# Kernel tuning notes

Measured on AMD Instinct MI355X. Metric: run time of the kernel, lower is better.

The kernel has to match this reference:

```python
import jax, jax.numpy as jnp
import numpy as np

D_MODEL = 1024

def setup_inputs() -> dict:
    key = jax.random.key(0)
    k1, k2, k3, k4, k5 = jax.random.split(key, 5)
    x = jax.random.normal(k1, (4, 2048, D_MODEL), dtype=jnp.float32)
    # torch nn.Linear weights: [out_features, in_features]
    W_qkv = jax.random.normal(k2, (3 * D_MODEL, D_MODEL), dtype=jnp.float32) * (1.0 / np.sqrt(D_MODEL))
    b_qkv = jax.random.normal(k3, (3 * D_MODEL,), dtype=jnp.float32) * 0.01
    W_proj = jax.random.normal(k4, (D_MODEL, D_MODEL), dtype=jnp.float32) * (1.0 / np.sqrt(D_MODEL))
    b_proj = jax.random.normal(k5, (D_MODEL,), dtype=jnp.float32) * 0.01
    return {"x": x, "W_qkv": W_qkv, "b_qkv": b_qkv, "W_proj": W_proj, "b_proj": b_proj}

def reference(x, W_qkv, b_qkv, W_proj, b_proj):
    # qkv projection: x @ W.T + b  (torch Linear convention)
    qkv = jnp.einsum('bsd,ed->bse', x, W_qkv) + b_qkv  # [B,S,3D]
    q, k, v = jnp.split(qkv, 3, axis=-1)               # each [B,S,D]
    scale = 1.0 / jnp.sqrt(jnp.asarray(q.shape[-1], dtype=q.dtype))
    scores = jnp.einsum('bqd,bkd->bqk', q, k) * scale   # [B,S,S]
    attn = jax.nn.softmax(scores, axis=-1)
    out = jnp.einsum('bqk,bkd->bqd', attn, v)           # [B,S,D]
    return jnp.einsum('bsd,ed->bse', out, W_proj) + b_proj
```

## Files before the change

kernel.cpp:

```cpp
#include <hip/hip_runtime.h>
#include <stdint.h>
#include <stddef.h>


typedef __attribute__((ext_vector_type(8))) short bf16x8;
typedef __attribute__((ext_vector_type(4))) float f32x4;

__device__ __forceinline__ unsigned short f2bf(float f) {
  unsigned u = __float_as_uint(f);
  u += 0x7fffu + ((u >> 16) & 1u);
  return (unsigned short)(u >> 16);
}
__device__ __forceinline__ float bf2f(unsigned short h) {
  return __uint_as_float(((unsigned)h) << 16);
}

typedef const __attribute__((address_space(1))) void* gas_ptr;
typedef __attribute__((address_space(3))) void* las_ptr;

__device__ __forceinline__ void gload_lds16(const void* g, void* l) {
  __builtin_amdgcn_global_load_lds((gas_ptr)(uintptr_t)g,
                                   (las_ptr)(uint32_t)(uintptr_t)l, 16, 0, 0);
}

__device__ __forceinline__ f32x4 mfma16(bf16x8 a, bf16x8 b, f32x4 c) {
  return __builtin_amdgcn_mfma_f32_16x16x32_bf16(a, b, c, 0, 0, 0);
}

__global__ __launch_bounds__(256) void cvt_all(
    const float* __restrict__ x, unsigned short* __restrict__ xo,
    const float* __restrict__ wq, unsigned short* __restrict__ wqo,
    const float* __restrict__ wp, unsigned short* __restrict__ wpo) {
  const int NX = 8388608, NQ = 3145728, NP = 1048576;
  int i = (blockIdx.x * blockDim.x + threadIdx.x) * 4;
  int stride = gridDim.x * blockDim.x * 4;
  for (; i < NX + NQ + NP; i += stride) {
    const float* src;
    unsigned short* dst;
    int off;
    if (i < NX) { src = x; dst = xo; off = i; }
    else if (i < NX + NQ) { src = wq; dst = wqo; off = i - NX; }
    else { src = wp; dst = wpo; off = i - NX - NQ; }
    float4 v = *reinterpret_cast<const float4*>(src + off);
    ushort4 o;
    o.x = f2bf(v.x); o.y = f2bf(v.y); o.z = f2bf(v.z); o.w = f2bf(v.w);
    *reinterpret_cast<ushort4*>(dst + off) = o;
  }
}

__device__ __forceinline__ void stage_gf(const unsigned short* __restrict__ P,
                                         int ld, unsigned short* dst, int wid,
                                         int lane) {
#pragma unroll
  for (int c = 0; c < 4; ++c) {
    int s = (c * 4 + wid) * 64 + lane;
    int row = s >> 3, g = s & 7;
    gload_lds16(P + (size_t)row * ld + ((g ^ (row & 7)) * 8),
                dst + (c * 4 + wid) * 512);
  }
}

template <bool OUT_BF16, bool HAS_BIAS, bool EXPOUT, bool RINV, bool QKV>
__global__ __launch_bounds__(256, 2) void gf(
    const unsigned short* __restrict__ A, const unsigned short* __restrict__ B,
    void* __restrict__ Cv, void* __restrict__ Cv2,
    const float* __restrict__ bias,
    int K, int lda, int ldb, int ldc,
    long long strideA, long long strideB, long long strideC, float alpha) {
  __shared__ unsigned short lds[2][2][128 * 64];

  const int bz = blockIdx.z;
  const int gx = gridDim.x;
  int lin = blockIdx.y * gx + blockIdx.x;
  int bx, by;
  {
    const int nwg = gx * gridDim.y;
    const int q = nwg >> 3;
    lin = (lin & 7) * q + (lin >> 3);
    const int t = lin >> 6, r = lin & 63;
    const int tilesX = gx >> 3;
    bx = (t % tilesX) * 8 + (r & 7);
    by = (t / tilesX) * 8 + (r >> 3);
  }
  const int rowBase = by * 128;
  const int colBase = bx * 128;

  const unsigned short* Ap = A + (size_t)bz * (size_t)strideA + (size_t)rowBase * lda;
  const unsigned short* Bp = B + (size_t)bz * (size_t)strideB + (size_t)colBase * ldb;

  const int tid = threadIdx.x;
  const int wid = tid >> 6;
  const int lane = tid & 63;
  const int wr = wid >> 1;
  const int wc = wid & 1;
  const int fr = lane & 15;
  const int kgi = lane >> 4;

  const int nt = K >> 6;

  f32x4 acc[4][4] = {};
  f32x4 rsacc[4] = {};
  bf16x8 ones;
#pragma unroll
  for (int i = 0; i < 8; ++i) ones[i] = (short)0x3F80;

  stage_gf(Ap, lda, &lds[0][0][0], wid, lane);
  stage_gf(Bp, ldb, &lds[0][1][0], wid, lane);
  asm volatile("s_waitcnt vmcnt(0)" ::: "memory");
  __builtin_amdgcn_sched_barrier(0);
  __builtin_amdgcn_s_barrier();

  for (int t = 0; t < nt; ++t) {
    const int cur = t & 1;
    if (t + 1 < nt) {
      stage_gf(Ap + (size_t)(t + 1) * 64, lda, &lds[cur ^ 1][0][0], wid, lane);
      stage_gf(Bp + (size_t)(t + 1) * 64, ldb, &lds[cur ^ 1][1][0], wid, lane);
    }
    const unsigned short* sAc = &lds[cur][0][0];
    const unsigned short* sBc = &lds[cur][1][0];

    bf16x8 af[4][2], bv[4][2];
#pragma unroll
    for (int m = 0; m < 4; ++m) {
      int row = wr * 64 + m * 16 + fr;
      int r7 = row & 7;
      af[m][0] = *(const bf16x8*)&sAc[row * 64 + ((kgi ^ r7) * 8)];
      af[m][1] = *(const bf16x8*)&sAc[row * 64 + (((4 + kgi) ^ r7) * 8)];
    }
#pragma unroll
    for (int n = 0; n < 4; ++n) {
      int row = wc * 64 + n * 16 + fr;
      int r7 = row & 7;
      bv[n][0] = *(const bf16x8*)&sBc[row * 64 + ((kgi ^ r7) * 8)];
      bv[n][1] = *(const bf16x8*)&sBc[row * 64 + (((4 + kgi) ^ r7) * 8)];
    }
    asm volatile("s_waitcnt lgkmcnt(0)" ::: "memory");
    __builtin_amdgcn_sched_barrier(0);
    __builtin_amdgcn_s_setprio(1);
#pragma unroll
    for (int m = 0; m < 4; ++m)
#pragma unroll
      for (int n = 0; n < 4; ++n) {
        acc[m][n] = mfma16(af[m][0], bv[n][0], acc[m][n]);
        acc[m][n] = mfma16(af[m][1], bv[n][1], acc[m][n]);
      }
    if (RINV) {
#pragma unroll
      for (int m = 0; m < 4; ++m) {
        rsacc[m] = mfma16(af[m][0], ones, rsacc[m]);
        rsacc[m] = mfma16(af[m][1], ones, rsacc[m]);
      }
    }
    __builtin_amdgcn_s_setprio(0);
    __builtin_amdgcn_sched_barrier(0);
    asm volatile("s_waitcnt vmcnt(0)" ::: "memory");
    __builtin_amdgcn_sched_barrier(0);
    __builtin_amdgcn_s_barrier();
  }

  const int rg = (lane >> 4) * 4;
  const bool doTrans = QKV && (colBase >= 2048);

  if (doTrans) {
    unsigned short* cl = &lds[0][0][0];
#pragma unroll
    for (int m = 0; m < 4; ++m) {
      int rloc0 = wr * 64 + m * 16 + rg;
#pragma unroll
      for (int n = 0; n < 4; ++n) {
        int cloc = wc * 64 + n * 16 + fr;
        float bvs = HAS_BIAS ? bias[colBase + cloc] : 0.0f;
#pragma unroll
        for (int j = 0; j < 4; ++j) {
          float v = acc[m][n][j] * alpha + bvs;
          cl[cloc * 136 + rloc0 + j] = f2bf(v);
        }
      }
    }
    __syncthreads();
    const int b = rowBase >> 11;
    const int s0 = rowBase & 2047;
    const int dBase = colBase - 2048;
    unsigned short* Vt = reinterpret_cast<unsigned short*>(Cv2);
#pragma unroll
    for (int i = 0; i < 8; ++i) {
      int slot = i * 256 + tid;
      int d = slot >> 4, sg = slot & 15;
      bf16x8 v = *(const bf16x8*)&cl[d * 136 + sg * 8];
      *(bf16x8*)&Vt[((size_t)(b * 1024 + dBase + d)) * 2048 + s0 + sg * 8] = v;
    }
  } else if (OUT_BF16) {
    unsigned short* cl = &lds[0][0][0];
#pragma unroll
    for (int m = 0; m < 4; ++m) {
      int rloc0 = wr * 64 + m * 16 + rg;
      float rs4[4];
      if (RINV) {
#pragma unroll
        for (int j = 0; j < 4; ++j) rs4[j] = 1.0f / rsacc[m][j];
      }
#pragma unroll
      for (int n = 0; n < 4; ++n) {
        int cloc = wc * 64 + n * 16 + fr;
        float bvs = 0.0f;
        if (HAS_BIAS) bvs = bias[colBase + cloc];
#pragma unroll
        for (int j = 0; j < 4; ++j) {
          int row = rloc0 + j;
          float v = acc[m][n][j] * alpha;
          if (EXPOUT) v = __expf(v);
          else v += bvs;
          if (RINV) v *= rs4[j];
          int gW = cloc >> 3;
          int gS = (gW & 8) | ((gW & 7) ^ (row & 7));
          cl[row * 128 + gS * 8 + (cloc & 7)] = f2bf(v);
        }
      }
    }
    __syncthreads();
    unsigned short* Cb =
        reinterpret_cast<unsigned short*>(Cv) + (size_t)bz * (size_t)strideC;
#pragma unroll
    for (int i = 0; i < 8; ++i) {
      int slot = i * 256 + tid;
      int row = slot >> 4, g = slot & 15;
      int gS = (g & 8) | ((g & 7) ^ (row & 7));
      bf16x8 v = *(const bf16x8*)&cl[row * 128 + gS * 8];
      *(bf16x8*)&Cb[(size_t)(rowBase + row) * ldc + colBase + g * 8] = v;
    }
  } else {
    float* clf = reinterpret_cast<float*>(&lds[0][0][0]);
#pragma unroll
    for (int m = 0; m < 4; ++m) {
      int rloc0 = wr * 64 + m * 16 + rg;
#pragma unroll
      for (int n = 0; n < 4; ++n) {
        int cloc = wc * 64 + n * 16 + fr;
        float bvs = 0.0f;
        if (HAS_BIAS) bvs = bias[colBase + cloc];
#pragma unroll
        for (int j = 0; j < 4; ++j) {
          int row = rloc0 + j;
          float v = acc[m][n][j] * alpha + bvs;
          int gW = cloc >> 2;
          int gS = (gW & 24) | ((gW & 7) ^ (row & 7));
          clf[row * 128 + gS * 4 + (cloc & 3)] = v;
        }
      }
    }
    __syncthreads();
    float* Cf = reinterpret_cast<float*>(Cv) + (size_t)bz * (size_t)strideC;
#pragma unroll
    for (int i = 0; i < 16; ++i) {
      int slot = i * 256 + tid;
      int row = slot >> 5, g = slot & 31;
      int gS = (g & 24) | ((g & 7) ^ (row & 7));
      float4 v = *(const float4*)&clf[row * 128 + gS * 4];
      *(float4*)&Cf[(size_t)(rowBase + row) * ldc + colBase + g * 4] = v;
    }
  }
}

extern "C" void kernel_launch(void* const* d_in, const int* in_sizes, int n_in,
                              void* d_out, int out_size, void* d_ws, size_t ws_size,
                              hipStream_t stream) {
  const float* x     = (const float*)d_in[0];
  const float* Wqkv  = (const float*)d_in[1];
  const float* bqkv  = (const float*)d_in[2];
  const float* Wproj = (const float*)d_in[3];
  const float* bproj = (const float*)d_in[4];
  float* out = (float*)d_out;

  char* ws = (char*)d_ws;
  unsigned short* qk   = (unsigned short*)(ws + 0);
  unsigned short* xatt = (unsigned short*)(ws + 50331648);
  unsigned short* wq   = (unsigned short*)(ws + 67108864);
  unsigned short* wp   = (unsigned short*)(ws + 73400320);
  unsigned short* vt   = (unsigned short*)(ws + 75497472);
  unsigned short* sc   = (unsigned short*)(ws + 92274688);

  dim3 blk256(256);

  cvt_all<<<3072, blk256, 0, stream>>>(x, xatt, Wqkv, wq, Wproj, wp);

  gf<true, true, false, false, true><<<dim3(24, 64, 1), blk256, 0, stream>>>(
      xatt, wq, qk, vt, bqkv,
      1024, 1024, 1024, 2048, 0, 0, 0, 1.0f);

  gf<true, false, true, false, false><<<dim3(16, 16, 4), blk256, 0, stream>>>(
      qk, qk + 1024, sc, nullptr, nullptr,
      1024, 2048, 2048, 2048,
      2048LL * 2048, 2048LL * 2048, 2048LL * 2048, 0.03125f);

  gf<true, false, false, true, false><<<dim3(8, 16, 4), blk256, 0, stream>>>(
      sc, vt, xatt, nullptr, nullptr,
      2048, 2048, 2048, 1024,
      2048LL * 2048, 1024LL * 2048, 2048LL * 1024, 1.0f);

  gf<false, true, false, false, false><<<dim3(8, 64, 1), blk256, 0, stream>>>(
      xatt, wp, out, nullptr, bproj,
      1024, 1024, 1024, 1024, 0, 0, 0, 1.0f);
}
```

Before: 170.4 us.

## Add 256x256-tile 512-thread GEMM kernel for QKV and score stages

Introduces a new g256 kernel with 256x256 output tiles, 8 waves, and a 64 KB-per-buffer double-buffered LDS stage, and uses it for the QKV projection and the QK^T exp-score GEMM. The larger tile halves global/LDS traffic per FLOP compared with the 128x128 tiles. The V-transpose epilogue now uses a swizzled LDS layout instead of the padded one. The grid-swizzle is generalized to handle widths not divisible by 8. The cost is higher register pressure (8x4 accumulators per wave) and a much larger LDS footprint, 128 KB per block, which limits occupancy. Fewer blocks also risk tail effects, for example 384 blocks for QKV and 256 for scores.

```diff
diff --git a/kernel.cpp b/kernel.cpp
--- a/kernel.cpp
+++ b/kernel.cpp
@@ -48,26 +48,28 @@
   }
 }
 
-__device__ __forceinline__ void stage_gf(const unsigned short* __restrict__ P,
-                                         int ld, unsigned short* dst, int wid,
-                                         int lane) {
+__device__ __forceinline__ void stage_g256(const unsigned short* __restrict__ P,
+                                           int ld, unsigned short* dst,
+                                           int tid) {
+  const int wid = tid >> 6, lane = tid & 63;
 #pragma unroll
   for (int c = 0; c < 4; ++c) {
-    int s = (c * 4 + wid) * 64 + lane;
+    int s = c * 512 + tid;
     int row = s >> 3, g = s & 7;
     gload_lds16(P + (size_t)row * ld + ((g ^ (row & 7)) * 8),
-                dst + (c * 4 + wid) * 512);
-  }
-}
-
-template <bool OUT_BF16, bool HAS_BIAS, bool EXPOUT, bool RINV, bool QKV>
-__global__ __launch_bounds__(256, 2) void gf(
+                dst + (c * 512 + wid * 64) * 8);
+    (void)lane;
+  }
+}
+
+template <bool HAS_BIAS, bool EXPOUT, bool QKV_SPLIT>
+__global__ __launch_bounds__(512, 2) void g256(
     const unsigned short* __restrict__ A, const unsigned short* __restrict__ B,
     void* __restrict__ Cv, void* __restrict__ Cv2,
     const float* __restrict__ bias,
     int K, int lda, int ldb, int ldc,
     long long strideA, long long strideB, long long strideC, float alpha) {
-  __shared__ unsigned short lds[2][2][128 * 64];
+  __shared__ unsigned short lds[2][2][256 * 64];
 
   const int bz = blockIdx.z;
   const int gx = gridDim.x;
@@ -77,10 +79,193 @@
     const int nwg = gx * gridDim.y;
     const int q = nwg >> 3;
     lin = (lin & 7) * q + (lin >> 3);
-    const int t = lin >> 6, r = lin & 63;
-    const int tilesX = gx >> 3;
-    bx = (t % tilesX) * 8 + (r & 7);
-    by = (t / tilesX) * 8 + (r >> 3);
+    const int TW = (gx % 8 == 0) ? 8 : ((gx % 4 == 0) ? 4 : 1);
+    if (TW > 1) {
+      const int grp = TW * 8;
+      const int t = lin / grp, r = lin % grp;
+      const int tilesX = gx / TW;
+      bx = (t % tilesX) * TW + (r % TW);
+      by = (t / tilesX) * 8 + (r / TW);
+    } else {
+      bx = lin % gx; by = lin / gx;
+    }
+  }
+  const int rowBase = by * 256;
+  const int colBase = bx * 256;
+
+  const unsigned short* Ap = A + (size_t)bz * (size_t)strideA + (size_t)rowBase * lda;
+  const unsigned short* Bp = B + (size_t)bz * (size_t)strideB + (size_t)colBase * ldb;
+
+  const int tid = threadIdx.x;
+  const int wid = tid >> 6;
+  const int lane = tid & 63;
+  const int wr = wid >> 2;
+  const int wc = wid & 3;
+  const int fr = lane & 15;
+  const int kgi = lane >> 4;
+
+  const int nt = K >> 6;
+
+  f32x4 acc[8][4] = {};
+
+  stage_g256(Ap, lda, &lds[0][0][0], tid);
+  stage_g256(Bp, ldb, &lds[0][1][0], tid);
+  asm volatile("s_waitcnt vmcnt(0)" ::: "memory");
+  __builtin_amdgcn_sched_barrier(0);
+  __builtin_amdgcn_s_barrier();
+
+  for (int t = 0; t < nt; ++t) {
+    const int cur = t & 1;
+    if (t + 1 < nt) {
+      stage_g256(Ap + (size_t)(t + 1) * 64, lda, &lds[cur ^ 1][0][0], tid);
+      stage_g256(Bp + (size_t)(t + 1) * 64, ldb, &lds[cur ^ 1][1][0], tid);
+    }
+    const unsigned short* sAc = &lds[cur][0][0];
+    const unsigned short* sBc = &lds[cur][1][0];
+
+    bf16x8 af[8][2], bv[4][2];
+#pragma unroll
+    for (int m = 0; m < 8; ++m) {
+      int row = wr * 128 + m * 16 + fr;
+      int r7 = row & 7;
+      af[m][0] = *(const bf16x8*)&sAc[row * 64 + ((kgi ^ r7) * 8)];
+      af[m][1] = *(const bf16x8*)&sAc[row * 64 + (((4 + kgi) ^ r7) * 8)];
+    }
+#pragma unroll
+    for (int n = 0; n < 4; ++n) {
+      int row = wc * 64 + n * 16 + fr;
+      int r7 = row & 7;
+      bv[n][0] = *(const bf16x8*)&sBc[row * 64 + ((kgi ^ r7) * 8)];
+      bv[n][1] = *(const bf16x8*)&sBc[row * 64 + (((4 + kgi) ^ r7) * 8)];
+    }
+    asm volatile("s_waitcnt lgkmcnt(0)" ::: "memory");
+    __builtin_amdgcn_sched_barrier(0);
+    __builtin_amdgcn_s_setprio(1);
+#pragma unroll
+    for (int m = 0; m < 8; ++m)
+#pragma unroll
+      for (int n = 0; n < 4; ++n) {
+        acc[m][n] = mfma16(af[m][0], bv[n][0], acc[m][n]);
+        acc[m][n] = mfma16(af[m][1], bv[n][1], acc[m][n]);
+      }
+    __builtin_amdgcn_s_setprio(0);
+    __builtin_amdgcn_sched_barrier(0);
+    asm volatile("s_waitcnt vmcnt(0)" ::: "memory");
+    __builtin_amdgcn_sched_barrier(0);
+    __builtin_amdgcn_s_barrier();
+  }
+
+  __syncthreads();
+
+  const int rg = (lane >> 4) * 4;
+  const bool doTrans = QKV_SPLIT && (colBase >= 2048);
+
+  if (doTrans) {
+    unsigned short* cl = &lds[0][0][0];
+#pragma unroll
+    for (int m = 0; m < 8; ++m) {
+      int rloc0 = wr * 128 + m * 16 + rg;
+#pragma unroll
+      for (int n = 0; n < 4; ++n) {
+        int cloc = wc * 64 + n * 16 + fr;
+        float bvs = HAS_BIAS ? bias[colBase + cloc] : 0.0f;
+#pragma unroll
+        for (int j = 0; j < 4; ++j) {
+          int s = rloc0 + j;
+          float v = acc[m][n][j] * alpha + bvs;
+          int sg = s >> 3;
+          int gS = (sg & 24) | ((sg & 7) ^ (cloc & 7));
+          cl[cloc * 256 + gS * 8 + (s & 7)] = f2bf(v);
+        }
+      }
+    }
+    __syncthreads();
+    const int b = rowBase >> 11;
+    const int s0 = rowBase & 2047;
+    const int dBase = colBase - 2048;
+    unsigned short* Vt = reinterpret_cast<unsigned short*>(Cv2);
+#pragma unroll
+    for (int i = 0; i < 16; ++i) {
+      int slot = i * 512 + tid;
+      int d = slot >> 5, sg = slot & 31;
+      int gS = (sg & 24) | ((sg & 7) ^ (d & 7));
+      bf16x8 v = *(const bf16x8*)&cl[d * 256 + gS * 8];
+      *(bf16x8*)&Vt[((size_t)(b * 1024 + dBase + d)) * 2048 + s0 + sg * 8] = v;
+    }
+  } else {
+    unsigned short* cl = &lds[0][0][0];
+#pragma unroll
+    for (int m = 0; m < 8; ++m) {
+      int rloc0 = wr * 128 + m * 16 + rg;
+#pragma unroll
+      for (int n = 0; n < 4; ++n) {
+        int cloc = wc * 64 + n * 16 + fr;
+        float bvs = 0.0f;
+        if (HAS_BIAS) bvs = bias[colBase + cloc];
+#pragma unroll
+        for (int j = 0; j < 4; ++j) {
+          int row = rloc0 + j;
+          float v = acc[m][n][j] * alpha;
+          if (EXPOUT) v = __expf(v);
+          else v += bvs;
+          int gW = cloc >> 3;
+          int gS = (gW & 24) | ((gW & 7) ^ (row & 7));
+          cl[row * 256 + gS * 8 + (cloc & 7)] = f2bf(v);
+        }
+      }
+    }
+    __syncthreads();
+    unsigned short* Cb =
+        reinterpret_cast<unsigned short*>(Cv) + (size_t)bz * (size_t)strideC;
+#pragma unroll
+    for (int i = 0; i < 16; ++i) {
+      int slot = i * 512 + tid;
+      int row = slot >> 5, g = slot & 31;
+      int gS = (g & 24) | ((g & 7) ^ (row & 7));
+      bf16x8 v = *(const bf16x8*)&cl[row * 256 + gS * 8];
+      *(bf16x8*)&Cb[(size_t)(rowBase + row) * ldc + colBase + g * 8] = v;
+    }
+  }
+}
+
+__device__ __forceinline__ void stage_gf(const unsigned short* __restrict__ P,
+                                         int ld, unsigned short* dst, int wid,
+                                         int lane) {
+#pragma unroll
+  for (int c = 0; c < 4; ++c) {
+    int s = (c * 4 + wid) * 64 + lane;
+    int row = s >> 3, g = s & 7;
+    gload_lds16(P + (size_t)row * ld + ((g ^ (row & 7)) * 8),
+                dst + (c * 4 + wid) * 512);
+  }
+}
+
+template <bool OUT_BF16, bool HAS_BIAS, bool RINV>
+__global__ __launch_bounds__(256, 2) void gf(
+    const unsigned short* __restrict__ A, const unsigned short* __restrict__ B,
+    void* __restrict__ Cv, const float* __restrict__ bias,
+    int K, int lda, int ldb, int ldc,
+    long long strideA, long long strideB, long long strideC, float alpha) {
+  __shared__ unsigned short lds[2][2][128 * 64];
+
+  const int bz = blockIdx.z;
+  const int gx = gridDim.x;
+  int lin = blockIdx.y * gx + blockIdx.x;
+  int bx, by;
+  {
+    const int nwg = gx * gridDim.y;
+    const int q = nwg >> 3;
+    lin = (lin & 7) * q + (lin >> 3);
+    const int TW = (gx % 8 == 0) ? 8 : ((gx % 4 == 0) ? 4 : 1);
+    if (TW > 1 && (gridDim.y % 8) == 0) {
+      const int grp = TW * 8;
+      const int t = lin / grp, r = lin % grp;
+      const int tilesX = gx / TW;
+      bx = (t % tilesX) * TW + (r % TW);
+      by = (t / tilesX) * 8 + (r / TW);
+    } else {
+      bx = lin % gx; by = lin / gx;
+    }
   }
   const int rowBase = by * 128;
   const int colBase = bx * 128;
@@ -159,37 +344,8 @@
   }
 
   const int rg = (lane >> 4) * 4;
-  const bool doTrans = QKV && (colBase >= 2048);
-
-  if (doTrans) {
-    unsigned short* cl = &lds[0][0][0];
-#pragma unroll
-    for (int m = 0; m < 4; ++m) {
-      int rloc0 = wr * 64 + m * 16 + rg;
-#pragma unroll
-      for (int n = 0; n < 4; ++n) {
-        int cloc = wc * 64 + n * 16 + fr;
-        float bvs = HAS_BIAS ? bias[colBase + cloc] : 0.0f;
-#pragma unroll
-        for (int j = 0; j < 4; ++j) {
-          float v = acc[m][n][j] * alpha + bvs;
-          cl[cloc * 136 + rloc0 + j] = f2bf(v);
-        }
-      }
-    }
-    __syncthreads();
-    const int b = rowBase >> 11;
-    const int s0 = rowBase & 2047;
-    const int dBase = colBase - 2048;
-    unsigned short* Vt = reinterpret_cast<unsigned short*>(Cv2);
-#pragma unroll
-    for (int i = 0; i < 8; ++i) {
-      int slot = i * 256 + tid;
-      int d = slot >> 4, sg = slot & 15;
-      bf16x8 v = *(const bf16x8*)&cl[d * 136 + sg * 8];
-      *(bf16x8*)&Vt[((size_t)(b * 1024 + dBase + d)) * 2048 + s0 + sg * 8] = v;
-    }
-  } else if (OUT_BF16) {
+
+  if (OUT_BF16) {
     unsigned short* cl = &lds[0][0][0];
 #pragma unroll
     for (int m = 0; m < 4; ++m) {
@@ -207,9 +363,7 @@
 #pragma unroll
         for (int j = 0; j < 4; ++j) {
           int row = rloc0 + j;
-          float v = acc[m][n][j] * alpha;
-          if (EXPOUT) v = __expf(v);
-          else v += bvs;
+          float v = acc[m][n][j] * alpha + bvs;
           if (RINV) v *= rs4[j];
           int gW = cloc >> 3;
           int gS = (gW & 8) | ((gW & 7) ^ (row & 7));
@@ -279,25 +433,25 @@
   unsigned short* vt   = (unsigned short*)(ws + 75497472);
   unsigned short* sc   = (unsigned short*)(ws + 92274688);
 
-  dim3 blk256(256);
+  dim3 blk256(256), blk512(512);
 
   cvt_all<<<3072, blk256, 0, stream>>>(x, xatt, Wqkv, wq, Wproj, wp);
 
-  gf<true, true, false, false, true><<<dim3(24, 64, 1), blk256, 0, stream>>>(
+  g256<true, false, true><<<dim3(12, 32, 1), blk512, 0, stream>>>(
       xatt, wq, qk, vt, bqkv,
       1024, 1024, 1024, 2048, 0, 0, 0, 1.0f);
 
-  gf<true, false, true, false, false><<<dim3(16, 16, 4), blk256, 0, stream>>>(
+  g256<false, true, false><<<dim3(8, 8, 4), blk512, 0, stream>>>(
       qk, qk + 1024, sc, nullptr, nullptr,
       1024, 2048, 2048, 2048,
       2048LL * 2048, 2048LL * 2048, 2048LL * 2048, 0.03125f);
 
-  gf<true, false, false, true, false><<<dim3(8, 16, 4), blk256, 0, stream>>>(
-      sc, vt, xatt, nullptr, nullptr,
+  gf<true, false, true><<<dim3(8, 16, 4), blk256, 0, stream>>>(
+      sc, vt, xatt, nullptr,
       2048, 2048, 2048, 1024,
       2048LL * 2048, 1024LL * 2048, 2048LL * 1024, 1.0f);
 
-  gf<false, true, false, false, false><<<dim3(8, 64, 1), blk256, 0, stream>>>(
-      xatt, wp, out, nullptr, bproj,
+  gf<false, true, false><<<dim3(8, 64, 1), blk256, 0, stream>>>(
+      xatt, wp, out, bproj,
       1024, 1024, 1024, 1024, 0, 0, 0, 1.0f);
 }
```

After: 178.6 us. 4.8% more time.

## Load B operand straight from global into registers and raise occupancy

Applied to the files above, without the earlier changes.

The GEMM kernel stops staging the B tile in LDS. Each wave now reads its B fragments directly from global memory every K step, and only A stays double-buffered in LDS. This shrinks the LDS footprint so launch bounds can ask for three blocks per CU, and the fp32 epilogue is split into two unswizzled 64-row halves so it fits the smaller buffer. The cost is that B loads are no longer prefetched, so their global latency sits on the critical path unless occupancy hides it. The hand-tuned waitcnt, priority and scheduling barriers are also dropped, and the unswizzled fp32 epilogue may cause LDS bank conflicts.

```diff
diff --git a/kernel.cpp b/kernel.cpp
--- a/kernel.cpp
+++ b/kernel.cpp
@@ -48,9 +48,9 @@
   }
 }
 
-__device__ __forceinline__ void stage_gf(const unsigned short* __restrict__ P,
-                                         int ld, unsigned short* dst, int wid,
-                                         int lane) {
+__device__ __forceinline__ void stage_A(const unsigned short* __restrict__ P,
+                                        int ld, unsigned short* dst, int wid,
+                                        int lane) {
 #pragma unroll
   for (int c = 0; c < 4; ++c) {
     int s = (c * 4 + wid) * 64 + lane;
@@ -61,13 +61,13 @@
 }
 
 template <bool OUT_BF16, bool HAS_BIAS, bool EXPOUT, bool RINV, bool QKV>
-__global__ __launch_bounds__(256, 2) void gf(
+__global__ __launch_bounds__(256, 3) void gf(
     const unsigned short* __restrict__ A, const unsigned short* __restrict__ B,
     void* __restrict__ Cv, void* __restrict__ Cv2,
     const float* __restrict__ bias,
     int K, int lda, int ldb, int ldc,
     long long strideA, long long strideB, long long strideC, float alpha) {
-  __shared__ unsigned short lds[2][2][128 * 64];
+  __shared__ unsigned short lds[2][8704];
 
   const int bz = blockIdx.z;
   const int gx = gridDim.x;
@@ -104,22 +104,29 @@
 #pragma unroll
   for (int i = 0; i < 8; ++i) ones[i] = (short)0x3F80;
 
-  stage_gf(Ap, lda, &lds[0][0][0], wid, lane);
-  stage_gf(Bp, ldb, &lds[0][1][0], wid, lane);
-  asm volatile("s_waitcnt vmcnt(0)" ::: "memory");
-  __builtin_amdgcn_sched_barrier(0);
-  __builtin_amdgcn_s_barrier();
+  const unsigned short* Brow[4];
+#pragma unroll
+  for (int n = 0; n < 4; ++n)
+    Brow[n] = Bp + (size_t)(wc * 64 + n * 16 + fr) * ldb + kgi * 8;
+
+  stage_A(Ap, lda, &lds[0][0], wid, lane);
+  __syncthreads();
 
   for (int t = 0; t < nt; ++t) {
     const int cur = t & 1;
-    if (t + 1 < nt) {
-      stage_gf(Ap + (size_t)(t + 1) * 64, lda, &lds[cur ^ 1][0][0], wid, lane);
-      stage_gf(Bp + (size_t)(t + 1) * 64, ldb, &lds[cur ^ 1][1][0], wid, lane);
-    }
-    const unsigned short* sAc = &lds[cur][0][0];
-    const unsigned short* sBc = &lds[cur][1][0];
-
-    bf16x8 af[4][2], bv[4][2];
+    if (t + 1 < nt)
+      stage_A(Ap + (size_t)(t + 1) * 64, lda, &lds[cur ^ 1][0], wid, lane);
+
+    const int k0 = t * 64;
+    bf16x8 bv[4][2];
+#pragma unroll
+    for (int n = 0; n < 4; ++n) {
+      bv[n][0] = *(const bf16x8*)(Brow[n] + k0);
+      bv[n][1] = *(const bf16x8*)(Brow[n] + k0 + 32);
+    }
+
+    const unsigned short* sAc = &lds[cur][0];
+    bf16x8 af[4][2];
 #pragma unroll
     for (int m = 0; m < 4; ++m) {
       int row = wr * 64 + m * 16 + fr;
@@ -128,16 +135,6 @@
       af[m][1] = *(const bf16x8*)&sAc[row * 64 + (((4 + kgi) ^ r7) * 8)];
     }
 #pragma unroll
-    for (int n = 0; n < 4; ++n) {
-      int row = wc * 64 + n * 16 + fr;
-      int r7 = row & 7;
-      bv[n][0] = *(const bf16x8*)&sBc[row * 64 + ((kgi ^ r7) * 8)];
-      bv[n][1] = *(const bf16x8*)&sBc[row * 64 + (((4 + kgi) ^ r7) * 8)];
-    }
-    asm volatile("s_waitcnt lgkmcnt(0)" ::: "memory");
-    __builtin_amdgcn_sched_barrier(0);
-    __builtin_amdgcn_s_setprio(1);
-#pragma unroll
     for (int m = 0; m < 4; ++m)
 #pragma unroll
       for (int n = 0; n < 4; ++n) {
@@ -151,18 +148,14 @@
         rsacc[m] = mfma16(af[m][1], ones, rsacc[m]);
       }
     }
-    __builtin_amdgcn_s_setprio(0);
-    __builtin_amdgcn_sched_barrier(0);
-    asm volatile("s_waitcnt vmcnt(0)" ::: "memory");
-    __builtin_amdgcn_sched_barrier(0);
-    __builtin_amdgcn_s_barrier();
+    __syncthreads();
   }
 
   const int rg = (lane >> 4) * 4;
   const bool doTrans = QKV && (colBase >= 2048);
 
   if (doTrans) {
-    unsigned short* cl = &lds[0][0][0];
+    unsigned short* cl = &lds[0][0];
 #pragma unroll
     for (int m = 0; m < 4; ++m) {
       int rloc0 = wr * 64 + m * 16 + rg;
@@ -190,7 +183,7 @@
       *(bf16x8*)&Vt[((size_t)(b * 1024 + dBase + d)) * 2048 + s0 + sg * 8] = v;
     }
   } else if (OUT_BF16) {
-    unsigned short* cl = &lds[0][0][0];
+    unsigned short* cl = &lds[0][0];
 #pragma unroll
     for (int m = 0; m < 4; ++m) {
       int rloc0 = wr * 64 + m * 16 + rg;
@@ -229,34 +222,36 @@
       *(bf16x8*)&Cb[(size_t)(rowBase + row) * ldc + colBase + g * 8] = v;
     }
   } else {
-    float* clf = reinterpret_cast<float*>(&lds[0][0][0]);
-#pragma unroll
-    for (int m = 0; m < 4; ++m) {
-      int rloc0 = wr * 64 + m * 16 + rg;
-#pragma unroll
-      for (int n = 0; n < 4; ++n) {
-        int cloc = wc * 64 + n * 16 + fr;
-        float bvs = 0.0f;
-        if (HAS_BIAS) bvs = bias[colBase + cloc];
-#pragma unroll
-        for (int j = 0; j < 4; ++j) {
-          int row = rloc0 + j;
-          float v = acc[m][n][j] * alpha + bvs;
-          int gW = cloc >> 2;
-          int gS = (gW & 24) | ((gW & 7) ^ (row & 7));
-          clf[row * 128 + gS * 4 + (cloc & 3)] = v;
+    float* clf = reinterpret_cast<float*>(&lds[0][0]);
+    float* Cf = reinterpret_cast<float*>(Cv) + (size_t)bz * (size_t)strideC;
+#pragma unroll
+    for (int half = 0; half < 2; ++half) {
+      if (wr == half) {
+#pragma unroll
+        for (int m = 0; m < 4; ++m) {
+          int rloc0 = m * 16 + rg;
+#pragma unroll
+          for (int n = 0; n < 4; ++n) {
+            int cloc = wc * 64 + n * 16 + fr;
+            float bvs = 0.0f;
+            if (HAS_BIAS) bvs = bias[colBase + cloc];
+#pragma unroll
+            for (int j = 0; j < 4; ++j) {
+              float v = acc[m][n][j] * alpha + bvs;
+              clf[(rloc0 + j) * 128 + cloc] = v;
+            }
+          }
         }
       }
-    }
-    __syncthreads();
-    float* Cf = reinterpret_cast<float*>(Cv) + (size_t)bz * (size_t)strideC;
-#pragma unroll
-    for (int i = 0; i < 16; ++i) {
-      int slot = i * 256 + tid;
-      int row = slot >> 5, g = slot & 31;
-      int gS = (g & 24) | ((g & 7) ^ (row & 7));
-      float4 v = *(const float4*)&clf[row * 128 + gS * 4];
-      *(float4*)&Cf[(size_t)(rowBase + row) * ldc + colBase + g * 4] = v;
+      __syncthreads();
+#pragma unroll
+      for (int i = 0; i < 8; ++i) {
+        int slot = i * 256 + tid;
+        int row = slot >> 5, g = slot & 31;
+        float4 v = *(const float4*)&clf[row * 128 + g * 4];
+        *(float4*)&Cf[(size_t)(rowBase + half * 64 + row) * ldc + colBase + g * 4] = v;
+      }
+      __syncthreads();
     }
   }
 }
```

New measurement: 318.4 us. 86.8% more time.
